# Kernel tuning notes

Hardware: AMD Instinct MI355X
Metric: run time of the kernel (lower is better)

Reference implementation:

```python
import jax, jax.numpy as jnp
import numpy as np

N_NODES = 50000


def _inv_sqrt_deg(idx, n):
    # degree per node from an edge-endpoint index vector; 0-degree -> norm 0 (DGL behavior)
    deg = jax.ops.segment_sum(jnp.ones(idx.shape[0], jnp.float32), idx, num_segments=n)
    return jnp.where(deg > 0, jax.lax.rsqrt(jnp.maximum(deg, 1.0)), 0.0)


def _graph_conv(x, src, dst, W, b, norm_src, norm_dst, n):
    # DGL GraphConv, norm='both': D_dst^{-1/2} A D_src^{-1/2} X W + b
    h = (x * norm_src[:, None]) @ W            # [N, out]
    agg = jax.ops.segment_sum(h[src], dst, num_segments=n)  # SpMM via gather+scatter-add
    return agg * norm_dst[:, None] + b


def setup_inputs() -> dict:
    key = jax.random.key(0)
    ks = jax.random.split(key, 8)
    N, E, D, H, C = N_NODES, 800000, 64, 64, 10
    s = 1.0 / np.sqrt(H)
    return {
        "x": jax.random.normal(ks[0], (N, D), jnp.float32),
        "src": jax.random.randint(ks[1], (E,), 0, N, jnp.int32),
        "dst": jax.random.randint(ks[2], (E,), 0, N, jnp.int32),
        "W1": jax.random.normal(ks[3], (D, H), jnp.float32) * s,
        "b1": jnp.zeros((H,), jnp.float32),
        "W2": jax.random.normal(ks[4], (H, H), jnp.float32) * s,
        "b2": jnp.zeros((H,), jnp.float32),
        "W3": jax.random.normal(ks[5], (H, H), jnp.float32) * s,
        "b3": jnp.zeros((H,), jnp.float32),
        "Wfc": jax.random.normal(ks[6], (H, C), jnp.float32) * s,
        "bfc": jnp.zeros((C,), jnp.float32),
    }


def reference(x, src, dst, W1, b1, W2, b2, W3, b3, Wfc, bfc):
    n = x.shape[0]
    norm_src = _inv_sqrt_deg(src, n)  # out-degree^{-1/2}
    norm_dst = _inv_sqrt_deg(dst, n)  # in-degree^{-1/2}
    h = jnp.tanh(_graph_conv(x, src, dst, W1, b1, norm_src, norm_dst, n))
    h = jnp.tanh(_graph_conv(h, src, dst, W2, b2, norm_src, norm_dst, n))
    h = jnp.tanh(_graph_conv(h, src, dst, W3, b3, norm_src, norm_dst, n))
    return h @ Wfc + bfc
```

## Files before the change

### kernel.cpp

```cpp
#include <hip/hip_runtime.h>
#include <hip/hip_fp16.h>
#include <math.h>

#define THREADS 256
#define CHUNK_SHIFT 15
#define CHUNK (1 << CHUNK_SHIFT)
#define LDS_WORDS 12500
#define MAXB 16
#define XS_STRIDE 68

__global__ __launch_bounds__(1024)
void k_hist(const int* __restrict__ src, const int* __restrict__ dst,
            unsigned int* __restrict__ partS, unsigned int* __restrict__ partD,
            unsigned char* __restrict__ rank, unsigned int* __restrict__ counter,
            int E, int P, int words) {
    __shared__ unsigned int hist[LDS_WORDS];
    if (blockIdx.x == 0 && threadIdx.x == 0) *counter = 0u;
    int isSrc = (blockIdx.x >= (unsigned)P);
    int b = isSrc ? (blockIdx.x - P) : blockIdx.x;
    int tid = threadIdx.x;

    for (int w = tid; w < words; w += 1024) hist[w] = 0u;
    __syncthreads();

    int start = b << CHUNK_SHIFT;
    int end = start + CHUNK; if (end > E) end = E;

    if (isSrc) {
        for (int e = start + tid; e < end; e += 1024) {
            int s = src[e];
            atomicAdd(&hist[s >> 2], 1u << ((s & 3) * 8));
        }
    } else {
        for (int e = start + tid; e < end; e += 1024) {
            int d = dst[e];
            unsigned int old = atomicAdd(&hist[d >> 2], 1u << ((d & 3) * 8));
            rank[e] = (unsigned char)((old >> ((d & 3) * 8)) & 0xFFu);
        }
    }
    __syncthreads();

    unsigned int* part = isSrc ? partS : partD;
    for (int w = tid; w < words; w += 1024)
        part[(size_t)b * words + w] = hist[w];
}

__global__ __launch_bounds__(THREADS)
void k_pre(const unsigned int* __restrict__ partS,
           const unsigned int* __restrict__ partD,
           unsigned int* __restrict__ prefD,
           int* __restrict__ deg_d, float* __restrict__ ns, float* __restrict__ nd,
           int* __restrict__ rp, int* __restrict__ bsum,
           unsigned int* __restrict__ counter,
           int P, int words, int N) {
    __shared__ unsigned int qsD[4][64];
    __shared__ unsigned int qsS[4][64];
    int t = threadIdx.x;
    int widx = t & 63;
    int q = t >> 6;
    int w = blockIdx.x * 64 + widx;
    bool valid = (w < words);

    int per = (P + 3) >> 2;
    int blo = q * per;
    int cnt = P - blo; if (cnt > per) cnt = per; if (cnt < 0) cnt = 0;

    unsigned int vD[MAXB];
    unsigned int runD = 0, runS = 0;
#pragma unroll
    for (int bb = 0; bb < MAXB; bb++) {
        unsigned int vd = 0, vs = 0;
        if (bb < cnt && valid) {
            size_t off = (size_t)(blo + bb) * words + w;
            vd = partD[off];
            vs = partS[off];
        }
        vD[bb] = vd;
        runD += vd;
        runS += vs;
    }
    qsD[q][widx] = runD;
    qsS[q][widx] = runS;
    __syncthreads();

    unsigned int baseD = 0, totD = 0, totS = 0;
#pragma unroll
    for (int qq = 0; qq < 4; qq++) {
        unsigned int xd = qsD[qq][widx];
        unsigned int xs = qsS[qq][widx];
        if (qq < q) baseD += xd;
        totD += xd;
        totS += xs;
    }

    unsigned int pref = baseD;
#pragma unroll
    for (int bb = 0; bb < MAXB; bb++) {
        if (bb < cnt && valid)
            prefD[(size_t)(blo + bb) * words + w] = pref;
        pref += vD[bb];
    }

    if (q == 0) {
        int b0 = (int)(totD & 0xFFu), b1 = (int)((totD >> 8) & 0xFFu),
            b2 = (int)((totD >> 16) & 0xFFu), b3 = (int)((totD >> 24) & 0xFFu);
        int wsum = b0 + b1 + b2 + b3;
        int incl = wsum;
#pragma unroll
        for (int off = 1; off < 64; off <<= 1) {
            int y = __shfl_up(incl, off);
            if (widx >= off) incl += y;
        }
        int excl = incl - wsum;
        int btot = __shfl(incl, 63);
        if (widx == 0)
            bsum[blockIdx.x] = (int)atomicAdd(counter, (unsigned int)btot);
        if (valid) {
            int s0 = (int)(totS & 0xFFu), s1 = (int)((totS >> 8) & 0xFFu),
                s2 = (int)((totS >> 16) & 0xFFu), s3 = (int)((totS >> 24) & 0xFFu);
            int4 dv; dv.x = b0; dv.y = b1; dv.z = b2; dv.w = b3;
            *(int4*)&deg_d[(size_t)4 * w] = dv;
            float4 ndv;
            ndv.x = b0 ? 1.0f / sqrtf((float)b0) : 0.0f;
            ndv.y = b1 ? 1.0f / sqrtf((float)b1) : 0.0f;
            ndv.z = b2 ? 1.0f / sqrtf((float)b2) : 0.0f;
            ndv.w = b3 ? 1.0f / sqrtf((float)b3) : 0.0f;
            *(float4*)&nd[(size_t)4 * w] = ndv;
            float4 nsv;
            nsv.x = s0 ? 1.0f / sqrtf((float)s0) : 0.0f;
            nsv.y = s1 ? 1.0f / sqrtf((float)s1) : 0.0f;
            nsv.z = s2 ? 1.0f / sqrtf((float)s2) : 0.0f;
            nsv.w = s3 ? 1.0f / sqrtf((float)s3) : 0.0f;
            *(float4*)&ns[(size_t)4 * w] = nsv;
            int4 rv; rv.x = excl; rv.y = excl + b0;
            rv.z = excl + b0 + b1; rv.w = excl + b0 + b1 + b2;
            *(int4*)&rp[(size_t)4 * w] = rv;
        }
    }
}

__global__ __launch_bounds__(256, 4)
void k_fill_gemm(const int* __restrict__ src, const int* __restrict__ dst,
                 const int* __restrict__ rp, const int* __restrict__ bsum,
                 const unsigned char* __restrict__ rank,
                 const unsigned int* __restrict__ prefD,
                 int* __restrict__ col, int E, int words, int gFill,
                 const float* __restrict__ X, const float* __restrict__ norm,
                 const float* __restrict__ W, __half* __restrict__ H, int N) {
    __shared__ float Xs[64 * XS_STRIDE];
    __shared__ float Ws[64 * 64];
    int tid = threadIdx.x;

    if ((int)blockIdx.x < gFill) {
        int e = blockIdx.x * 256 + tid;
        if (e < E) {
            int d = dst[e];
            int b = e >> CHUNK_SHIFT;
            unsigned int pk = prefD[(size_t)b * words + (d >> 2)];
            int pref = (int)((pk >> ((d & 3) * 8)) & 0xFFu);
            col[rp[d] + bsum[d >> 8] + pref + (int)rank[e]] = src[e];
        }
        return;
    }

    int rowBase = ((int)blockIdx.x - gFill) * 64;
    for (int i = tid; i < 1024; i += 256)
        ((float4*)Ws)[i] = ((const float4*)W)[i];
    for (int i = tid; i < 1024; i += 256) {
        int r  = i >> 4;
        int k4 = i & 15;
        int row = rowBase + r;
        float4 v = make_float4(0.f, 0.f, 0.f, 0.f);
        if (row < N) {
            v = ((const float4*)X)[(size_t)row * 16 + k4];
            float nv = norm[row];
            v.x *= nv; v.y *= nv; v.z *= nv; v.w *= nv;
        }
        *((float4*)&Xs[r * XS_STRIDE + (k4 << 2)]) = v;
    }
    __syncthreads();

    int tc = tid & 15;
    int tr = tid >> 4;
    int c0 = tc * 4, r0 = tr * 4;
    float acc[4][4] = {};

#pragma unroll 2
    for (int k = 0; k < 64; k += 4) {
        float4 wv[4];
#pragma unroll
        for (int kk = 0; kk < 4; kk++)
            wv[kk] = *((const float4*)&Ws[(k + kk) * 64 + c0]);
#pragma unroll
        for (int j = 0; j < 4; j++) {
            float4 xv = *((const float4*)&Xs[(r0 + j) * XS_STRIDE + k]);
            acc[j][0] += xv.x * wv[0].x; acc[j][1] += xv.x * wv[0].y;
            acc[j][2] += xv.x * wv[0].z; acc[j][3] += xv.x * wv[0].w;
            acc[j][0] += xv.y * wv[1].x; acc[j][1] += xv.y * wv[1].y;
            acc[j][2] += xv.y * wv[1].z; acc[j][3] += xv.y * wv[1].w;
            acc[j][0] += xv.z * wv[2].x; acc[j][1] += xv.z * wv[2].y;
            acc[j][2] += xv.z * wv[2].z; acc[j][3] += xv.z * wv[2].w;
            acc[j][0] += xv.w * wv[3].x; acc[j][1] += xv.w * wv[3].y;
            acc[j][2] += xv.w * wv[3].z; acc[j][3] += xv.w * wv[3].w;
        }
    }
#pragma unroll
    for (int j = 0; j < 4; j++) {
        int row = rowBase + r0 + j;
        if (row < N) {
            __half2 h01 = __floats2half2_rn(acc[j][0], acc[j][1]);
            __half2 h23 = __floats2half2_rn(acc[j][2], acc[j][3]);
            uint2 pk;
            pk.x = *(unsigned int*)&h01;
            pk.y = *(unsigned int*)&h23;
            *((uint2*)(H + (size_t)row * 64 + c0)) = pk;
        }
    }
}

template<int FC>
__global__ __launch_bounds__(256, 4)
void k_agg_gemm(const uint4* __restrict__ H4, const int* __restrict__ rp,
                const int* __restrict__ bsum, const int* __restrict__ deg,
                const int* __restrict__ col, const float* __restrict__ nd,
                const float* __restrict__ nsrc, const float* __restrict__ bias,
                const float* __restrict__ W, const float* __restrict__ Wb2,
                void* __restrict__ OutP, int N) {
    __shared__ float Xs[64 * XS_STRIDE];
    __shared__ float Ws[FC ? 640 : 4096];
    __shared__ float Wb[16];
    int tid = threadIdx.x;

    if constexpr (FC == 0) {
        for (int i = tid; i < 1024; i += 256)
            ((float4*)Ws)[i] = ((const float4*)W)[i];
    } else {
        for (int i = tid; i < 640; i += 256) {
            int k = i / 10, c = i - k * 10;
            Ws[c * 64 + k] = W[i];
        }
        if (tid < 10) Wb[tid] = Wb2[tid];
    }

    int wave = tid >> 6;
    int lane = tid & 63;
    int g = lane >> 3;
    int l = lane & 7;
    int rowBase = blockIdx.x * 64;

    float4 bv0 = *((const float4*)&bias[l * 8]);
    float4 bv1 = *((const float4*)&bias[l * 8 + 4]);

    int nodeA = rowBase + wave * 16 + g;
    int nodeB = nodeA + 8;

    int stA = 0, nA = 0; float nvA = 0.f, nsA = 0.f;
    if (nodeA < N) {
        stA = rp[nodeA] + bsum[nodeA >> 8];
        nA  = deg[nodeA];
        nvA = nd[nodeA];
        if constexpr (FC == 0) nsA = nsrc[nodeA];
    }
    int stB = 0, nB = 0; float nvB = 0.f, nsB = 0.f;
    if (nodeB < N) {
        stB = rp[nodeB] + bsum[nodeB >> 8];
        nB  = deg[nodeB];
        nvB = nd[nodeB];
        if constexpr (FC == 0) nsB = nsrc[nodeB];
    }

    int idxA = (l < nA) ? col[stA + l] : 0;
    int idxB = (l < nB) ? col[stB + l] : 0;

    int mA = nA, mB = nB;
#pragma unroll
    for (int d = 8; d <= 32; d <<= 1) {
        int tA = __shfl_xor(mA, d); mA = mA > tA ? mA : tA;
        int tB = __shfl_xor(mB, d); mB = mB > tB ? mB : tB;
    }

    auto run = [&](int start, int n, int m, int idx, float nv, float nsv,
                   bool vn, int row) {
        float acc[8] = {0.f, 0.f, 0.f, 0.f, 0.f, 0.f, 0.f, 0.f};
        for (int j0 = 0; j0 < m; j0 += 8) {
            int idxn = ((j0 + 8 + l) < n) ? col[start + j0 + 8 + l] : 0;
#pragma unroll
            for (int jj = 0; jj < 8; jj++) {
                int s = __shfl(idx, (g << 3) + jj);
                if (j0 + jj < n) {
                    uint4 v = H4[(size_t)s * 8 + l];
                    float2 f0 = __half22float2(*(__half2*)&v.x);
                    float2 f1 = __half22float2(*(__half2*)&v.y);
                    float2 f2 = __half22float2(*(__half2*)&v.z);
                    float2 f3 = __half22float2(*(__half2*)&v.w);
                    acc[0] += f0.x; acc[1] += f0.y; acc[2] += f1.x; acc[3] += f1.y;
                    acc[4] += f2.x; acc[5] += f2.y; acc[6] += f3.x; acc[7] += f3.y;
                }
            }
            idx = idxn;
        }
        float4 o0, o1;
        o0.x = tanhf(acc[0] * nv + bv0.x);
        o0.y = tanhf(acc[1] * nv + bv0.y);
        o0.z = tanhf(acc[2] * nv + bv0.z);
        o0.w = tanhf(acc[3] * nv + bv0.w);
        o1.x = tanhf(acc[4] * nv + bv1.x);
        o1.y = tanhf(acc[5] * nv + bv1.y);
        o1.z = tanhf(acc[6] * nv + bv1.z);
        o1.w = tanhf(acc[7] * nv + bv1.w);
        if constexpr (FC == 0) {
            o0.x *= nsv; o0.y *= nsv; o0.z *= nsv; o0.w *= nsv;
            o1.x *= nsv; o1.y *= nsv; o1.z *= nsv; o1.w *= nsv;
        }
        if (!vn) {
            o0 = make_float4(0.f, 0.f, 0.f, 0.f);
            o1 = make_float4(0.f, 0.f, 0.f, 0.f);
        }
        *((float4*)&Xs[row * XS_STRIDE + l * 8])     = o0;
        *((float4*)&Xs[row * XS_STRIDE + l * 8 + 4]) = o1;
    };

    run(stA, nA, mA, idxA, nvA, nsA, nodeA < N, wave * 16 + g);
    run(stB, nB, mB, idxB, nvB, nsB, nodeB < N, wave * 16 + 8 + g);
    __syncthreads();

    if constexpr (FC == 0) {
        __half* Hh = (__half*)OutP;
        int tc = tid & 15;
        int tr = tid >> 4;
        int c0 = tc * 4, r0 = tr * 4;
        float acc[4][4] = {};

#pragma unroll 2
        for (int k = 0; k < 64; k += 4) {
            float4 wv[4];
#pragma unroll
            for (int kk = 0; kk < 4; kk++)
                wv[kk] = *((const float4*)&Ws[(k + kk) * 64 + c0]);
#pragma unroll
            for (int j = 0; j < 4; j++) {
                float4 xv = *((const float4*)&Xs[(r0 + j) * XS_STRIDE + k]);
                acc[j][0] += xv.x * wv[0].x; acc[j][1] += xv.x * wv[0].y;
                acc[j][2] += xv.x * wv[0].z; acc[j][3] += xv.x * wv[0].w;
                acc[j][0] += xv.y * wv[1].x; acc[j][1] += xv.y * wv[1].y;
                acc[j][2] += xv.y * wv[1].z; acc[j][3] += xv.y * wv[1].w;
                acc[j][0] += xv.z * wv[2].x; acc[j][1] += xv.z * wv[2].y;
                acc[j][2] += xv.z * wv[2].z; acc[j][3] += xv.z * wv[2].w;
                acc[j][0] += xv.w * wv[3].x; acc[j][1] += xv.w * wv[3].y;
                acc[j][2] += xv.w * wv[3].z; acc[j][3] += xv.w * wv[3].w;
            }
        }
#pragma unroll
        for (int j = 0; j < 4; j++) {
            int row = rowBase + r0 + j;
            if (row < N) {
                __half2 h01 = __floats2half2_rn(acc[j][0], acc[j][1]);
                __half2 h23 = __floats2half2_rn(acc[j][2], acc[j][3]);
                uint2 pk;
                pk.x = *(unsigned int*)&h01;
                pk.y = *(unsigned int*)&h23;
                *((uint2*)(Hh + (size_t)row * 64 + c0)) = pk;
            }
        }
    } else {
        float* outF = (float*)OutP;
        for (int idx = tid; idx < 640; idx += 256) {
            int ln = idx / 10;
            int cl = idx - ln * 10;
            float acc = Wb[cl];
#pragma unroll
            for (int k = 0; k < 64; k += 4) {
                float4 xv = *((const float4*)&Xs[ln * XS_STRIDE + k]);
                float4 wv = *((const float4*)&Ws[cl * 64 + k]);
                acc += xv.x * wv.x;
                acc += xv.y * wv.y;
                acc += xv.z * wv.z;
                acc += xv.w * wv.w;
            }
            int row = rowBase + ln;
            if (row < N) outF[(size_t)row * 10 + cl] = acc;
        }
    }
}

extern "C" void kernel_launch(void* const* d_in, const int* in_sizes, int n_in,
                              void* d_out, int out_size, void* d_ws, size_t ws_size,
                              hipStream_t stream) {
    const float* x   = (const float*)d_in[0];
    const int*   src = (const int*)d_in[1];
    const int*   dst = (const int*)d_in[2];
    const float* W1  = (const float*)d_in[3];
    const float* b1  = (const float*)d_in[4];
    const float* W2  = (const float*)d_in[5];
    const float* b2  = (const float*)d_in[6];
    const float* W3  = (const float*)d_in[7];
    const float* b3  = (const float*)d_in[8];
    const float* Wfc = (const float*)d_in[9];
    const float* bfc = (const float*)d_in[10];
    float* out = (float*)d_out;
    int N = in_sizes[0] / 64;
    int E = in_sizes[1];
    int P = (E + CHUNK - 1) >> CHUNK_SHIFT;
    int words = (N + 3) / 4;

    char* ws = (char*)d_ws;
    size_t p = 0;
    auto alloc = [&](size_t bytes) -> void* {
        void* r = ws + p;
        p = (p + bytes + 255) & ~(size_t)255;
        return r;
    };
    int*    deg_d = (int*)alloc((size_t)N * 4);
    int*    rp    = (int*)alloc((size_t)N * 4);
    int*    bsum  = (int*)alloc((size_t)THREADS * 4);
    unsigned char* rank = (unsigned char*)alloc((size_t)E);
    int*    col   = (int*)alloc((size_t)E * 4);
    float*  ns    = (float*)alloc((size_t)N * 4);
    float*  nd    = (float*)alloc((size_t)N * 4);
    unsigned int* partS = (unsigned int*)alloc((size_t)P * words * 4);
    unsigned int* partD = (unsigned int*)alloc((size_t)P * words * 4);
    unsigned int* prefD = (unsigned int*)alloc((size_t)P * words * 4);
    __half* bufH  = (__half*)alloc((size_t)N * 64 * 2);
    __half* bufH2 = (__half*)alloc((size_t)N * 64 * 2);
    unsigned int* counter = (unsigned int*)alloc(4);
    (void)ws_size; (void)n_in; (void)out_size;

    int gFill = (E + 255) / 256;
    int gP = (words + 63) / 64;
    int gG = (N + 63) / 64;

    k_hist<<<2 * P, 1024, 0, stream>>>(src, dst, partS, partD, rank, counter, E, P, words);
    k_pre <<<gP, THREADS, 0, stream>>>(partS, partD, prefD, deg_d, ns, nd,
                                       rp, bsum, counter, P, words, N);
    k_fill_gemm<<<gFill + gG, 256, 0, stream>>>(src, dst, rp, bsum, rank, prefD,
                                                col, E, words, gFill,
                                                x, ns, W1, bufH, N);
    k_agg_gemm<0><<<gG, 256, 0, stream>>>((const uint4*)bufH,  rp, bsum, deg_d, col,
                                          nd, ns, b1, W2, nullptr, bufH2, N);
    k_agg_gemm<0><<<gG, 256, 0, stream>>>((const uint4*)bufH2, rp, bsum, deg_d, col,
                                          nd, ns, b2, W3, nullptr, bufH, N);
    k_agg_gemm<1><<<gG, 256, 0, stream>>>((const uint4*)bufH,  rp, bsum, deg_d, col,
                                          nd, ns, b3, Wfc, bfc, out, N);
}
```

Before: 214.8 us.

## Split fp16 feature buffer into two column halves to shrink gather working set

Stores the hidden-feature matrix as two planar halves of 32 columns each instead of 64-column rows. The aggregation then runs twice per node, one pass per half, so each pass gathers from a smaller table that fits better in cache. Column-index loads are made nontemporal. The cost is reading the CSR column indices twice and running twice as many loop iterations, each with narrower 8-byte loads.

Result: slower. 266.5 us (+24.1%).

```diff
diff --git a/kernel.cpp b/kernel.cpp
--- a/kernel.cpp
+++ b/kernel.cpp
@@ -8,6 +8,7 @@
 #define LDS_WORDS 12500
 #define MAXB 16
 #define XS_STRIDE 68
+
 
 __global__ __launch_bounds__(1024)
 void k_hist(const int* __restrict__ src, const int* __restrict__ dst,
@@ -167,8 +168,7 @@
     for (int i = tid; i < 1024; i += 256)
         ((float4*)Ws)[i] = ((const float4*)W)[i];
     for (int i = tid; i < 1024; i += 256) {
-        int r  = i >> 4;
-        int k4 = i & 15;
+        int r = i >> 4, k4 = i & 15;
         int row = rowBase + r;
         float4 v = make_float4(0.f, 0.f, 0.f, 0.f);
         if (row < N) {
@@ -180,8 +180,7 @@
     }
     __syncthreads();
 
-    int tc = tid & 15;
-    int tr = tid >> 4;
+    int tc = tid & 15, tr = tid >> 4;
     int c0 = tc * 4, r0 = tr * 4;
     float acc[4][4] = {};
 
@@ -204,6 +203,8 @@
             acc[j][2] += xv.w * wv[3].z; acc[j][3] += xv.w * wv[3].w;
         }
     }
+    __half* Hh = H + (tc >= 8 ? (size_t)N * 32 : (size_t)0);
+    int cc = c0 & 31;
 #pragma unroll
     for (int j = 0; j < 4; j++) {
         int row = rowBase + r0 + j;
@@ -213,14 +214,14 @@
             uint2 pk;
             pk.x = *(unsigned int*)&h01;
             pk.y = *(unsigned int*)&h23;
-            *((uint2*)(H + (size_t)row * 64 + c0)) = pk;
+            *((uint2*)(Hh + (size_t)row * 32 + cc)) = pk;
         }
     }
 }
 
 template<int FC>
 __global__ __launch_bounds__(256, 4)
-void k_agg_gemm(const uint4* __restrict__ H4, const int* __restrict__ rp,
+void k_agg_gemm(const __half* __restrict__ Hbase, const int* __restrict__ rp,
                 const int* __restrict__ bsum, const int* __restrict__ deg,
                 const int* __restrict__ col, const float* __restrict__ nd,
                 const float* __restrict__ nsrc, const float* __restrict__ bias,
@@ -248,9 +249,6 @@
     int l = lane & 7;
     int rowBase = blockIdx.x * 64;
 
-    float4 bv0 = *((const float4*)&bias[l * 8]);
-    float4 bv1 = *((const float4*)&bias[l * 8 + 4]);
-
     int nodeA = rowBase + wave * 16 + g;
     int nodeB = nodeA + 8;
 
@@ -269,9 +267,6 @@
         if constexpr (FC == 0) nsB = nsrc[nodeB];
     }
 
-    int idxA = (l < nA) ? col[stA + l] : 0;
-    int idxB = (l < nB) ? col[stB + l] : 0;
-
     int mA = nA, mB = nB;
 #pragma unroll
     for (int d = 8; d <= 32; d <<= 1) {
@@ -279,55 +274,57 @@
         int tB = __shfl_xor(mB, d); mB = mB > tB ? mB : tB;
     }
 
-    auto run = [&](int start, int n, int m, int idx, float nv, float nsv,
+    float4 bvp0 = *((const float4*)&bias[l * 4]);
+    float4 bvp1 = *((const float4*)&bias[32 + l * 4]);
+
+    auto run = [&](const uint2* __restrict__ H2, float4 bv, int xb,
+                   int start, int n, int m, float nv, float nsv,
                    bool vn, int row) {
-        float acc[8] = {0.f, 0.f, 0.f, 0.f, 0.f, 0.f, 0.f, 0.f};
+        int idx = (l < n) ? __builtin_nontemporal_load(&col[start + l]) : 0;
+        float acc[4] = {0.f, 0.f, 0.f, 0.f};
         for (int j0 = 0; j0 < m; j0 += 8) {
-            int idxn = ((j0 + 8 + l) < n) ? col[start + j0 + 8 + l] : 0;
+            int idxn = ((j0 + 8 + l) < n)
+                     ? __builtin_nontemporal_load(&col[start + j0 + 8 + l]) : 0;
 #pragma unroll
             for (int jj = 0; jj < 8; jj++) {
                 int s = __shfl(idx, (g << 3) + jj);
                 if (j0 + jj < n) {
-                    uint4 v = H4[(size_t)s * 8 + l];
+                    uint2 v = H2[(size_t)s * 8 + l];
                     float2 f0 = __half22float2(*(__half2*)&v.x);
                     float2 f1 = __half22float2(*(__half2*)&v.y);
-                    float2 f2 = __half22float2(*(__half2*)&v.z);
-                    float2 f3 = __half22float2(*(__half2*)&v.w);
-                    acc[0] += f0.x; acc[1] += f0.y; acc[2] += f1.x; acc[3] += f1.y;
-                    acc[4] += f2.x; acc[5] += f2.y; acc[6] += f3.x; acc[7] += f3.y;
+                    acc[0] += f0.x; acc[1] += f0.y;
+                    acc[2] += f1.x; acc[3] += f1.y;
                 }
             }
             idx = idxn;
         }
-        float4 o0, o1;
-        o0.x = tanhf(acc[0] * nv + bv0.x);
-        o0.y = tanhf(acc[1] * nv + bv0.y);
-        o0.z = tanhf(acc[2] * nv + bv0.z);
-        o0.w = tanhf(acc[3] * nv + bv0.w);
-        o1.x = tanhf(acc[4] * nv + bv1.x);
-        o1.y = tanhf(acc[5] * nv + bv1.y);
-        o1.z = tanhf(acc[6] * nv + bv1.z);
-        o1.w = tanhf(acc[7] * nv + bv1.w);
+        float4 o;
+        o.x = tanhf(acc[0] * nv + bv.x);
+        o.y = tanhf(acc[1] * nv + bv.y);
+        o.z = tanhf(acc[2] * nv + bv.z);
+        o.w = tanhf(acc[3] * nv + bv.w);
         if constexpr (FC == 0) {
-            o0.x *= nsv; o0.y *= nsv; o0.z *= nsv; o0.w *= nsv;
-            o1.x *= nsv; o1.y *= nsv; o1.z *= nsv; o1.w *= nsv;
-        }
-        if (!vn) {
-            o0 = make_float4(0.f, 0.f, 0.f, 0.f);
-            o1 = make_float4(0.f, 0.f, 0.f, 0.f);
-        }
-        *((float4*)&Xs[row * XS_STRIDE + l * 8])     = o0;
-        *((float4*)&Xs[row * XS_STRIDE + l * 8 + 4]) = o1;
+            o.x *= nsv; o.y *= nsv; o.z *= nsv; o.w *= nsv;
+        }
+        if (!vn) o = make_float4(0.f, 0.f, 0.f, 0.f);
+        *((float4*)&Xs[row * XS_STRIDE + xb + l * 4]) = o;
     };
 
-    run(stA, nA, mA, idxA, nvA, nsA, nodeA < N, wave * 16 + g);
-    run(stB, nB, mB, idxB, nvB, nsB, nodeB < N, wave * 16 + 8 + g);
+    {
+        const uint2* H2 = (const uint2*)Hbase;
+        run(H2, bvp0, 0,  stA, nA, mA, nvA, nsA, nodeA < N, wave * 16 + g);
+        run(H2, bvp0, 0,  stB, nB, mB, nvB, nsB, nodeB < N, wave * 16 + 8 + g);
+    }
+    {
+        const uint2* H2 = (const uint2*)(Hbase + (size_t)N * 32);
+        run(H2, bvp1, 32, stA, nA, mA, nvA, nsA, nodeA < N, wave * 16 + g);
+        run(H2, bvp1, 32, stB, nB, mB, nvB, nsB, nodeB < N, wave * 16 + 8 + g);
+    }
     __syncthreads();
 
     if constexpr (FC == 0) {
-        __half* Hh = (__half*)OutP;
-        int tc = tid & 15;
-        int tr = tid >> 4;
+        __half* Hout = (__half*)OutP;
+        int tc = tid & 15, tr = tid >> 4;
         int c0 = tc * 4, r0 = tr * 4;
         float acc[4][4] = {};
 
@@ -350,6 +347,8 @@
                 acc[j][2] += xv.w * wv[3].z; acc[j][3] += xv.w * wv[3].w;
             }
         }
+        __half* Hh = Hout + (tc >= 8 ? (size_t)N * 32 : (size_t)0);
+        int cc = c0 & 31;
 #pragma unroll
         for (int j = 0; j < 4; j++) {
             int row = rowBase + r0 + j;
@@ -359,7 +358,7 @@
                 uint2 pk;
                 pk.x = *(unsigned int*)&h01;
                 pk.y = *(unsigned int*)&h23;
-                *((uint2*)(Hh + (size_t)row * 64 + c0)) = pk;
+                *((uint2*)(Hh + (size_t)row * 32 + cc)) = pk;
             }
         }
     } else {
@@ -372,10 +371,7 @@
             for (int k = 0; k < 64; k += 4) {
                 float4 xv = *((const float4*)&Xs[ln * XS_STRIDE + k]);
                 float4 wv = *((const float4*)&Ws[cl * 64 + k]);
-                acc += xv.x * wv.x;
-                acc += xv.y * wv.y;
-                acc += xv.z * wv.z;
-                acc += xv.w * wv.w;
+                acc += xv.x * wv.x + xv.y * wv.y + xv.z * wv.z + xv.w * wv.w;
             }
             int row = rowBase + ln;
             if (row < N) outF[(size_t)row * 10 + cl] = acc;
@@ -435,10 +431,10 @@
     k_fill_gemm<<<gFill + gG, 256, 0, stream>>>(src, dst, rp, bsum, rank, prefD,
                                                 col, E, words, gFill,
                                                 x, ns, W1, bufH, N);
-    k_agg_gemm<0><<<gG, 256, 0, stream>>>((const uint4*)bufH,  rp, bsum, deg_d, col,
+    k_agg_gemm<0><<<gG, 256, 0, stream>>>(bufH,  rp, bsum, deg_d, col,
                                           nd, ns, b1, W2, nullptr, bufH2, N);
-    k_agg_gemm<0><<<gG, 256, 0, stream>>>((const uint4*)bufH2, rp, bsum, deg_d, col,
+    k_agg_gemm<0><<<gG, 256, 0, stream>>>(bufH2, rp, bsum, deg_d, col,
                                           nd, ns, b2, W3, nullptr, bufH, N);
-    k_agg_gemm<1><<<gG, 256, 0, stream>>>((const uint4*)bufH,  rp, bsum, deg_d, col,
+    k_agg_gemm<1><<<gG, 256, 0, stream>>>(bufH,  rp, bsum, deg_d, col,
                                           nd, ns, b3, Wfc, bfc, out, N);
 }
```
